# Optimization experiments

Hardware: AMD Instinct MI355X
Metric: run time of the kernel (lower is better)

Reference implementation:

```python
import jax, jax.numpy as jnp
import numpy as np

# Faithful math of the torch module (dropout in eval mode => identity):
#   alpha = sigmoid(smoothing_weight)                       # [h,1] -> [1,1,h,1]
#   out[t] = alpha^(t+1) * v0 + sum_{s<=t} (1-alpha) alpha^(t-s) * values[s]
#   aux path kernel: weight/clamp(1-alpha,1e-6)*alpha => factor*alpha^(t-s+1)
#     with factor = (1-alpha)/max(1-alpha,1e-6) (== 1 unless alpha ~ 1)
# The torch code realizes this causal linear recurrence via FFT cross-correlation;
# here we use an associative (parallel) scan, which computes the same sums.

B, T, H, D = 8, 4096, 8, 64

def setup_inputs() -> dict:
    key = jax.random.key(0)
    k1, k2, k3, k4 = jax.random.split(key, 4)
    values = jax.random.normal(k1, (B, T, H, D), dtype=jnp.float32)
    aux_values = jax.random.normal(k2, (B, T, H, D), dtype=jnp.float32)
    v0 = jax.random.normal(k3, (1, 1, H, D), dtype=jnp.float32)
    smoothing_weight = jax.random.normal(k4, (H, 1), dtype=jnp.float32)
    return {"values": values, "aux_values": aux_values, "v0": v0,
            "smoothing_weight": smoothing_weight}

def reference(values, aux_values, v0, smoothing_weight):
    b, t, h, d = values.shape
    alpha = jax.nn.sigmoid(smoothing_weight).reshape(1, 1, h, 1)  # [1,1,h,1]
    one_m = 1.0 - alpha
    factor = one_m / jnp.maximum(one_m, 1e-6)  # == 1 unless alpha ~ 1 (clamp in torch)
    # Linear recurrence y[t] = alpha*y[t-1] + u[t], y[-1] = v0, where
    # u[t] = (1-alpha)*values[t] + factor*alpha*aux_values[t] (fused main + aux path).
    a = jnp.broadcast_to(alpha, (1, t, h, 1))               # decay coeffs
    u = one_m * values + (factor * alpha) * aux_values      # [b,t,h,d]
    def combine(c1, c2):
        a1, b1 = c1
        a2, b2 = c2
        return (a1 * a2, a2 * b1 + b2)
    A, Bsum = jax.lax.associative_scan(combine, (a, u), axis=1)
    # A[t] = alpha^(t+1); Bsum[t] = sum_{s<=t} alpha^(t-s) * u[s]
    return A * v0 + Bsum
```

## Files before the change

kernel.cpp:

```cpp
#include <hip/hip_runtime.h>
#include <math.h>

#define BB 8
#define TT 4096
#define HH 8
#define NCV 512
#define LCV (TT / NCV)
#define GRID (BB * NCV)

typedef float f32x4 __attribute__((ext_vector_type(4)));

__device__ __forceinline__ float sigmoidf_(float x) {
    return 1.0f / (1.0f + expf(-x));
}

__global__ __launch_bounds__(128, 8)
void k_agg(const float4* __restrict__ vals, const float4* __restrict__ aux,
           const float* __restrict__ w, float4* __restrict__ Z) {
    const int blk = blockIdx.x;
    const int b = blk >> 9;
    const int c = blk & (NCV - 1);
    const int tid = threadIdx.x;
    const int h = tid >> 4;

    const float alpha = sigmoidf_(w[h]);
    const float onem  = 1.0f - alpha;
    const float fa    = (onem / fmaxf(onem, 1e-6f)) * alpha;

    const int base = (b * TT + c * LCV) * 128 + tid;

    float4 v[LCV], a[LCV];
#pragma unroll
    for (int i = 0; i < LCV; ++i) v[i] = vals[base + i * 128];
#pragma unroll
    for (int i = 0; i < LCV; ++i) a[i] = aux[base + i * 128];

    float4 yy = make_float4(0.f, 0.f, 0.f, 0.f);
#pragma unroll
    for (int i = 0; i < LCV; ++i) {
        yy.x = alpha * yy.x + onem * v[i].x + fa * a[i].x;
        yy.y = alpha * yy.y + onem * v[i].y + fa * a[i].y;
        yy.z = alpha * yy.z + onem * v[i].z + fa * a[i].z;
        yy.w = alpha * yy.w + onem * v[i].w + fa * a[i].w;
    }
    Z[(b * NCV + c) * 128 + tid] = yy;
}

__global__ __launch_bounds__(NCV)
void k_scan(float4* __restrict__ ZP, const float* __restrict__ v0,
            const float* __restrict__ w) {
    __shared__ float lds[NCV][9];

    const int blk = blockIdx.x;
    const int b  = blk >> 6;
    const int h  = (blk >> 3) & 7;
    const int d8 = blk & 7;
    const int r4 = h * 16 + d8 * 2;
    const int tid = threadIdx.x;

    const float alpha = sigmoidf_(w[h]);
    const float aL = powf(alpha, (float)LCV);

    {
        float4 z0 = ZP[(b * NCV + tid) * 128 + r4];
        float4 z1 = ZP[(b * NCV + tid) * 128 + r4 + 1];
        lds[tid][0] = z0.x; lds[tid][1] = z0.y; lds[tid][2] = z0.z; lds[tid][3] = z0.w;
        lds[tid][4] = z1.x; lds[tid][5] = z1.y; lds[tid][6] = z1.z; lds[tid][7] = z1.w;
    }
    __syncthreads();

    const int c = tid;
    float s[8];
#pragma unroll
    for (int k = 0; k < 8; ++k) s[k] = lds[c][k];

    float m = aL;
    for (int off = 1; off < NCV; off <<= 1) {
        float tmp[8];
        const bool act = (c >= off);
        if (act) {
#pragma unroll
            for (int k = 0; k < 8; ++k) tmp[k] = lds[c - off][k];
        }
        __syncthreads();
        if (act) {
#pragma unroll
            for (int k = 0; k < 8; ++k) { s[k] += m * tmp[k]; lds[c][k] = s[k]; }
        }
        m *= m;
        __syncthreads();
    }

    const float pc = powf(alpha, (float)(LCV * c));
    const float4* v04 = (const float4*)v0;
#pragma unroll
    for (int k = 0; k < 2; ++k) {
        float4 vv = v04[r4 + k];
        float4 pr;
        if (c == 0) {
            pr = vv;
        } else {
            pr.x = pc * vv.x + lds[c - 1][k * 4 + 0];
            pr.y = pc * vv.y + lds[c - 1][k * 4 + 1];
            pr.z = pc * vv.z + lds[c - 1][k * 4 + 2];
            pr.w = pc * vv.w + lds[c - 1][k * 4 + 3];
        }
        ZP[(b * NCV + c) * 128 + r4 + k] = pr;
    }
}

__global__ __launch_bounds__(128, 8)
void k_out(const float4* __restrict__ vals, const float4* __restrict__ aux,
           const float* __restrict__ w, const float4* __restrict__ P,
           float4* __restrict__ out) {
    const int blk = blockIdx.x;
    const int b = blk >> 9;
    const int c = blk & (NCV - 1);
    const int tid = threadIdx.x;
    const int h = tid >> 4;

    const float alpha = sigmoidf_(w[h]);
    const float onem  = 1.0f - alpha;
    const float fa    = (onem / fmaxf(onem, 1e-6f)) * alpha;

    const float4 p = P[(b * NCV + c) * 128 + tid];
    const int base = (b * TT + c * LCV) * 128 + tid;

    float4 v[LCV], a[LCV];
#pragma unroll
    for (int i = 0; i < LCV; ++i) v[i] = vals[base + i * 128];
#pragma unroll
    for (int i = 0; i < LCV; ++i) a[i] = aux[base + i * 128];

    float4 yy = make_float4(0.f, 0.f, 0.f, 0.f);
    float coef = alpha;
#pragma unroll
    for (int i = 0; i < LCV; ++i) {
        yy.x = alpha * yy.x + onem * v[i].x + fa * a[i].x;
        yy.y = alpha * yy.y + onem * v[i].y + fa * a[i].y;
        yy.z = alpha * yy.z + onem * v[i].z + fa * a[i].z;
        yy.w = alpha * yy.w + onem * v[i].w + fa * a[i].w;
        float4 o;
        o.x = yy.x + coef * p.x;
        o.y = yy.y + coef * p.y;
        o.z = yy.z + coef * p.z;
        o.w = yy.w + coef * p.w;
        __builtin_nontemporal_store(*(const f32x4*)&o, (f32x4*)&out[base + i * 128]);
        coef *= alpha;
    }
}

extern "C" void kernel_launch(void* const* d_in, const int* in_sizes, int n_in,
                              void* d_out, int out_size, void* d_ws, size_t ws_size,
                              hipStream_t stream) {
    const float4* vals = (const float4*)d_in[0];
    const float4* aux  = (const float4*)d_in[1];
    const float*  v0   = (const float*)d_in[2];
    const float*  w    = (const float*)d_in[3];
    float4* out = (float4*)d_out;

    float4* ZP = (float4*)d_ws;

    k_agg <<<GRID, 128, 0, stream>>>(vals, aux, w, ZP);
    k_scan<<<BB * HH * 8, NCV, 0, stream>>>(ZP, v0, w);
    k_out <<<GRID, 128, 0, stream>>>(vals, aux, w, ZP, out);
}
```

Before: 209.7 us.

## Store local partial scan to output, then apply carry in a light final pass

```diff
diff --git a/kernel.cpp b/kernel.cpp
--- a/kernel.cpp
+++ b/kernel.cpp
@@ -14,9 +14,10 @@
     return 1.0f / (1.0f + expf(-x));
 }
 
-__global__ __launch_bounds__(128, 8)
-void k_agg(const float4* __restrict__ vals, const float4* __restrict__ aux,
-           const float* __restrict__ w, float4* __restrict__ Z) {
+__global__ __launch_bounds__(128)
+void k_partial(const f32x4* __restrict__ vals, const f32x4* __restrict__ aux,
+               const float* __restrict__ w, f32x4* __restrict__ out,
+               f32x4* __restrict__ Z) {
     const int blk = blockIdx.x;
     const int b = blk >> 9;
     const int c = blk & (NCV - 1);
@@ -29,21 +30,18 @@
 
     const int base = (b * TT + c * LCV) * 128 + tid;
 
-    float4 v[LCV], a[LCV];
-#pragma unroll
-    for (int i = 0; i < LCV; ++i) v[i] = vals[base + i * 128];
-#pragma unroll
-    for (int i = 0; i < LCV; ++i) a[i] = aux[base + i * 128];
-
-    float4 yy = make_float4(0.f, 0.f, 0.f, 0.f);
+    f32x4 y; y.x = 0.f; y.y = 0.f; y.z = 0.f; y.w = 0.f;
 #pragma unroll
     for (int i = 0; i < LCV; ++i) {
-        yy.x = alpha * yy.x + onem * v[i].x + fa * a[i].x;
-        yy.y = alpha * yy.y + onem * v[i].y + fa * a[i].y;
-        yy.z = alpha * yy.z + onem * v[i].z + fa * a[i].z;
-        yy.w = alpha * yy.w + onem * v[i].w + fa * a[i].w;
+        f32x4 v = vals[base + i * 128];
+        f32x4 a = aux[base + i * 128];
+        y.x = alpha * y.x + onem * v.x + fa * a.x;
+        y.y = alpha * y.y + onem * v.y + fa * a.y;
+        y.z = alpha * y.z + onem * v.z + fa * a.z;
+        y.w = alpha * y.w + onem * v.w + fa * a.w;
+        out[base + i * 128] = y;
     }
-    Z[(b * NCV + c) * 128 + tid] = yy;
+    Z[(b * NCV + c) * 128 + tid] = y;
 }
 
 __global__ __launch_bounds__(NCV)
@@ -109,10 +107,9 @@
     }
 }
 
-__global__ __launch_bounds__(128, 8)
-void k_out(const float4* __restrict__ vals, const float4* __restrict__ aux,
-           const float* __restrict__ w, const float4* __restrict__ P,
-           float4* __restrict__ out) {
+__global__ __launch_bounds__(128)
+void k_final(const float* __restrict__ w, const f32x4* __restrict__ P,
+             f32x4* __restrict__ out) {
     const int blk = blockIdx.x;
     const int b = blk >> 9;
     const int c = blk & (NCV - 1);
@@ -120,32 +117,18 @@
     const int h = tid >> 4;
 
     const float alpha = sigmoidf_(w[h]);
-    const float onem  = 1.0f - alpha;
-    const float fa    = (onem / fmaxf(onem, 1e-6f)) * alpha;
-
-    const float4 p = P[(b * NCV + c) * 128 + tid];
+    const f32x4 p = P[(b * NCV + c) * 128 + tid];
     const int base = (b * TT + c * LCV) * 128 + tid;
 
-    float4 v[LCV], a[LCV];
-#pragma unroll
-    for (int i = 0; i < LCV; ++i) v[i] = vals[base + i * 128];
-#pragma unroll
-    for (int i = 0; i < LCV; ++i) a[i] = aux[base + i * 128];
-
-    float4 yy = make_float4(0.f, 0.f, 0.f, 0.f);
     float coef = alpha;
 #pragma unroll
     for (int i = 0; i < LCV; ++i) {
-        yy.x = alpha * yy.x + onem * v[i].x + fa * a[i].x;
-        yy.y = alpha * yy.y + onem * v[i].y + fa * a[i].y;
-        yy.z = alpha * yy.z + onem * v[i].z + fa * a[i].z;
-        yy.w = alpha * yy.w + onem * v[i].w + fa * a[i].w;
-        float4 o;
-        o.x = yy.x + coef * p.x;
-        o.y = yy.y + coef * p.y;
-        o.z = yy.z + coef * p.z;
-        o.w = yy.w + coef * p.w;
-        __builtin_nontemporal_store(*(const f32x4*)&o, (f32x4*)&out[base + i * 128]);
+        f32x4 o = out[base + i * 128];
+        o.x += coef * p.x;
+        o.y += coef * p.y;
+        o.z += coef * p.z;
+        o.w += coef * p.w;
+        __builtin_nontemporal_store(o, &out[base + i * 128]);
         coef *= alpha;
     }
 }
@@ -153,15 +136,15 @@
 extern "C" void kernel_launch(void* const* d_in, const int* in_sizes, int n_in,
                               void* d_out, int out_size, void* d_ws, size_t ws_size,
                               hipStream_t stream) {
-    const float4* vals = (const float4*)d_in[0];
-    const float4* aux  = (const float4*)d_in[1];
-    const float*  v0   = (const float*)d_in[2];
-    const float*  w    = (const float*)d_in[3];
-    float4* out = (float4*)d_out;
+    const f32x4* vals = (const f32x4*)d_in[0];
+    const f32x4* aux  = (const f32x4*)d_in[1];
+    const float* v0   = (const float*)d_in[2];
+    const float* w    = (const float*)d_in[3];
+    f32x4* out = (f32x4*)d_out;
 
-    float4* ZP = (float4*)d_ws;
+    f32x4* ZP = (f32x4*)d_ws;
 
-    k_agg <<<GRID, 128, 0, stream>>>(vals, aux, w, ZP);
-    k_scan<<<BB * HH * 8, NCV, 0, stream>>>(ZP, v0, w);
-    k_out <<<GRID, 128, 0, stream>>>(vals, aux, w, ZP, out);
+    k_partial<<<GRID, 128, 0, stream>>>(vals, aux, w, out, ZP);
+    k_scan<<<BB * HH * 8, NCV, 0, stream>>>((float4*)ZP, v0, w);
+    k_final<<<GRID, 128, 0, stream>>>(w, ZP, out);
 }
```

After: 204.5 us. 1.03x faster.
